# Performance work log

Hardware: AMD Instinct MI355X
Metric: run time of the kernel (lower is better)

Reference implementation:

```python
import jax, jax.numpy as jnp
import numpy as np

N = 4096       # nodes
NFEAT = 256    # feature dim
NCLASS = 16
E = 65536      # edges = N * avg_degree(16)
NLAYER = 4
ALPHA = 0.5    # blancealpha (non-trainable)
LAMBDA_1 = 1.0
LAMBDA_2 = 1.0
EPS = 1e-12    # F.normalize eps


def setup_inputs() -> dict:
    key = jax.random.key(0)
    ks = jax.random.split(key, 9)
    feat = jax.random.normal(ks[0], (N, NFEAT), dtype=jnp.float32)
    z0 = jax.random.uniform(ks[1], (N, NFEAT), dtype=jnp.float32)       # torch.rand init of z
    w1 = jax.random.uniform(ks[2], (N, N), dtype=jnp.float32)           # uniform_(0,1)
    EA = jax.random.uniform(ks[3], (N, N), dtype=jnp.float32)           # uniform_(0,1)
    w2_w = jax.random.normal(ks[4], (2 * NFEAT, NCLASS), dtype=jnp.float32) * 0.05
    w2_b = jnp.zeros((NCLASS,), dtype=jnp.float32)
    edge_i = jax.random.randint(ks[5], (E,), 0, N, dtype=jnp.int32)
    edge_j = jax.random.randint(ks[6], (E,), 0, N, dtype=jnp.int32)
    edge_val = jax.random.uniform(ks[7], (E,), dtype=jnp.float32)
    # dense adjacency from the sparse edge list (coalesce -> duplicate indices sum)
    adj = jnp.zeros((N, N), dtype=jnp.float32).at[edge_i, edge_j].add(edge_val)
    # w22 = ones with zeros at edge positions (as in __init__)
    w22 = jnp.ones((N, N), dtype=jnp.float32).at[edge_i, edge_j].set(0.0)
    return dict(feat=feat, z0=z0, w1=w1, EA=EA, w2_w=w2_w, w2_b=w2_b,
                adj=adj, w22=w22, edge_val=edge_val, edge_i=edge_i, edge_j=edge_j)


def reference(feat, z0, w1, EA, w2_w, w2_b, adj, w22, edge_val, edge_i, edge_j):
    n = feat.shape[0]
    y = feat                      # y starts as feat
    z = z0                        # torch.rand init, passed in for determinism
    EP = jnp.ones((n, n), dtype=feat.dtype)
    masked_EA = ALPHA * EA * w22  # constant across layers
    for _ in range(NLAYER):
        # dropout is identity in eval mode (training=False)
        A = adj * EP + masked_EA            # [n, n]
        yyT = y @ y.T                       # [n, n] (reused; same values as the two torch.mm calls)
        temp = EP.T @ y + A @ y - yyT @ y   # [n, nfeat]
        temp = jax.nn.sigmoid(w1 @ temp)
        y_n = (LAMBDA_2 / 2) * temp + feat
        z_n = z - A @ z                     # (I - A) @ z
        # ans(z, adj): edgewise ||z_i - z_j|| * adj_val scattered to dense
        P = jnp.linalg.norm(z[edge_i] - z[edge_j], axis=1) * edge_val   # [E]
        M = jnp.zeros((n, n), dtype=z.dtype).at[edge_i, edge_j].add(P)
        EP = (LAMBDA_2 * (yyT - masked_EA) - LAMBDA_1 * 0.5 * M) / LAMBDA_2
        y, z = y_n, z_n
    # F.normalize(p=2, dim=1)
    y = y / jnp.maximum(jnp.linalg.norm(y, axis=1, keepdims=True), EPS)
    z = z / jnp.maximum(jnp.linalg.norm(z, axis=1, keepdims=True), EPS)
    p = jnp.concatenate([z, y], axis=1)     # [n, 2*nfeat]
    logits = p @ w2_w + w2_b
    return jax.nn.log_softmax(logits, axis=1)
```

## Files before the change

### kernel.cpp

```cpp
#include <hip/hip_runtime.h>

#define Nn 4096
#define Ff 256
#define NCLS 16
#define Ne 65536
#define TSZ 262144
#define NF (Nn*Ff)
#define NNx (Nn*Nn)
#define KS 4

typedef unsigned short u16;
typedef unsigned int u32;
typedef __attribute__((ext_vector_type(8))) short short8;
typedef __attribute__((ext_vector_type(4))) float float4v;

__device__ __forceinline__ float bfh(u16 u){ return __uint_as_float(((u32)u)<<16); }
__device__ __forceinline__ u16 f2bf(float f){
    u32 u = __float_as_uint(f);
    return (u16)((u + 0x7FFFu + ((u>>16)&1u)) >> 16);
}
__device__ __forceinline__ void gload16(const u16* g, u16* l){
    __builtin_amdgcn_global_load_lds(
        (const __attribute__((address_space(1))) u32*)(const void*)g,
        (__attribute__((address_space(3))) u32*)(void*)l, 16, 0, 0);
}

__device__ float g_yA[NF], g_yB[NF], g_zA[NF], g_zB[NF], g_t1[NF], g_T1[NF];
__device__ float g_Gp[16*Ff*Ff], g_col[Ff], g_P[Ne], g_cc[Ne], g_hV[TSZ];
__device__ float g_pb[(size_t)KS*NF];
__device__ u32 g_hK[TSZ], g_slot[Ne];
__device__ int g_cntI[Nn], g_cntJ[Nn], g_rpI[Nn+1], g_rpJ[Nn+1], g_fI[Nn], g_fJ[Nn];
__device__ int g_lI[Ne], g_lJ[Ne];
__device__ __align__(16) u16 g_w1h[NNx], g_w1l[NNx];
__device__ __align__(16) u16 g_meh[NNx], g_mel[NNx];
__device__ __align__(16) u16 g_mth[NNx], g_mtl[NNx];
__device__ __align__(16) u16 g_x0h[NF], g_x0l[NF], g_x1h[NF], g_x1l[NF];
__device__ __align__(16) u16 g_zt0h[NF], g_zt0l[NF], g_zt1h[NF], g_zt1l[NF];
__device__ __align__(16) u16 g_yr0h[NF], g_yr0l[NF], g_yr1h[NF], g_yr1l[NF];
__device__ __align__(16) u16 g_tth[NF], g_ttl[NF];
__device__ __align__(16) u16 g_gth[Ff*Ff], g_gtl[Ff*Ff];

__global__ __launch_bounds__(256) void k_zero(float* p, int n){
    int i = blockIdx.x*256 + threadIdx.x;
    if (i < n) p[i] = 0.f;
}
__global__ __launch_bounds__(256) void k_zeroi(int* p, int n){
    int i = blockIdx.x*256 + threadIdx.x;
    if (i < n) p[i] = 0;
}
__global__ __launch_bounds__(256) void k_fillc(float* p, float v, int n){
    int i = blockIdx.x*256 + threadIdx.x;
    if (i < n) p[i] = v;
}
__global__ __launch_bounds__(256) void k_hkeys_clear(u32* K){
    int i = blockIdx.x*256 + threadIdx.x;
    if (i < TSZ) K[i] = 0xFFFFFFFFu;
}
__global__ __launch_bounds__(256) void k_hsetup(u32* K, u32* slot, const int* ei, const int* ej){
    int e = blockIdx.x*256 + threadIdx.x;
    if (e >= Ne) return;
    u32 key = ((u32)ei[e] << 12) | (u32)ej[e];
    u32 h = (key * 2654435761u) & (TSZ-1);
    for (;;){
        u32 old = atomicCAS(&K[h], 0xFFFFFFFFu, key);
        if (old == 0xFFFFFFFFu || old == key){ slot[e] = h; break; }
        h = (h+1) & (TSZ-1);
    }
}

__global__ __launch_bounds__(256) void k_count(int* cntI, int* cntJ, const int* ei, const int* ej){
    int e = blockIdx.x*256 + threadIdx.x;
    if (e < Ne){ atomicAdd(&cntI[ei[e]], 1); atomicAdd(&cntJ[ej[e]], 1); }
}
__global__ __launch_bounds__(1024) void k_scan(const int* cnt, int* rp){
    __shared__ int s[1024];
    int t = threadIdx.x, b = t*4;
    int a0 = cnt[b], a1 = cnt[b+1], a2 = cnt[b+2], a3 = cnt[b+3];
    int sum = a0+a1+a2+a3;
    s[t] = sum; __syncthreads();
    for (int o = 1; o < 1024; o <<= 1){
        int v = (t >= o) ? s[t-o] : 0;
        __syncthreads();
        s[t] += v;
        __syncthreads();
    }
    int excl = s[t] - sum;
    rp[b] = excl; rp[b+1] = excl+a0; rp[b+2] = excl+a0+a1; rp[b+3] = excl+a0+a1+a2;
    if (t == 1023) rp[4096] = s[1023];
}
__global__ __launch_bounds__(256) void k_fillcsr(const int* rpI, const int* rpJ, int* fI, int* fJ,
                                                 int* lI, int* lJ, const int* ei, const int* ej){
    int e = blockIdx.x*256 + threadIdx.x;
    if (e >= Ne) return;
    int i = ei[e], j = ej[e];
    lI[rpI[i] + atomicAdd(&fI[i], 1)] = e;
    lJ[rpJ[j] + atomicAdd(&fJ[j], 1)] = e;
}

__global__ __launch_bounds__(256) void k_split4(ushort4* hi, ushort4* lo, const float4* w, int n4){
    int i = blockIdx.x*256 + threadIdx.x;
    if (i >= n4) return;
    float4 v = w[i];
    ushort4 h, l;
    h.x = f2bf(v.x); l.x = f2bf(v.x - bfh(h.x));
    h.y = f2bf(v.y); l.y = f2bf(v.y - bfh(h.y));
    h.z = f2bf(v.z); l.z = f2bf(v.z - bfh(h.z));
    h.w = f2bf(v.w); l.w = f2bf(v.w - bfh(h.w));
    hi[i] = h; lo[i] = l;
}
__global__ __launch_bounds__(256) void k_splitME2(u16* meh, u16* mel, u16* mth, u16* mtl,
                                                  const float* ea, const float* w22){
    __shared__ float T[64][65];
    int r0 = blockIdx.y*64, c0 = blockIdx.x*64;
    int c4 = threadIdx.x & 15, rr = threadIdx.x >> 4;
    for (int q = 0; q < 4; ++q){
        int r = q*16 + rr;
        size_t idx = (size_t)(r0+r)*Nn + c0 + c4*4;
        float4 e4 = *(const float4*)(ea + idx);
        float4 w4 = *(const float4*)(w22 + idx);
        float v0 = 0.5f*e4.x*w4.x, v1 = 0.5f*e4.y*w4.y, v2 = 0.5f*e4.z*w4.z, v3 = 0.5f*e4.w*w4.w;
        ushort4 h, l;
        h.x = f2bf(v0); l.x = f2bf(v0 - bfh(h.x));
        h.y = f2bf(v1); l.y = f2bf(v1 - bfh(h.y));
        h.z = f2bf(v2); l.z = f2bf(v2 - bfh(h.z));
        h.w = f2bf(v3); l.w = f2bf(v3 - bfh(h.w));
        *(ushort4*)(meh + idx) = h; *(ushort4*)(mel + idx) = l;
        T[r][c4*4+0] = v0; T[r][c4*4+1] = v1; T[r][c4*4+2] = v2; T[r][c4*4+3] = v3;
    }
    __syncthreads();
    for (int q = 0; q < 4; ++q){
        int oc = q*16 + rr;
        float v0 = T[c4*4+0][oc], v1 = T[c4*4+1][oc], v2 = T[c4*4+2][oc], v3 = T[c4*4+3][oc];
        ushort4 h, l;
        h.x = f2bf(v0); l.x = f2bf(v0 - bfh(h.x));
        h.y = f2bf(v1); l.y = f2bf(v1 - bfh(h.y));
        h.z = f2bf(v2); l.z = f2bf(v2 - bfh(h.z));
        h.w = f2bf(v3); l.w = f2bf(v3 - bfh(h.w));
        size_t o = (size_t)(c0+oc)*Nn + r0 + c4*4;
        *(ushort4*)(mth + o) = h; *(ushort4*)(mtl + o) = l;
    }
}
__global__ __launch_bounds__(256) void k_splitXT(u16* hi, u16* lo, const float* X){
    __shared__ float T[64][65];
    int r0 = blockIdx.y*64, c0 = blockIdx.x*64;
    int c = threadIdx.x & 63, rr = threadIdx.x >> 6;
    for (int q = 0; q < 16; ++q){
        int r = q*4 + rr;
        T[r][c] = X[(size_t)(r0+r)*Ff + c0 + c];
    }
    __syncthreads();
    for (int q = 0; q < 16; ++q){
        int r = q*4 + rr;
        float v = T[c][r];
        size_t o = (size_t)(c0+r)*Nn + r0 + c;
        u16 h = f2bf(v); hi[o] = h; lo[o] = f2bf(v - bfh(h));
    }
}
__global__ __launch_bounds__(256) void k_splitGT(u16* hi, u16* lo, const float* Gp){
    __shared__ float T[64][65];
    int r0 = blockIdx.y*64, c0 = blockIdx.x*64;
    int c = threadIdx.x & 63, rr = threadIdx.x >> 6;
    for (int q = 0; q < 16; ++q){
        int r = q*4 + rr;
        float v = 0.f;
        #pragma unroll
        for (int z = 0; z < 16; ++z) v += Gp[z*(Ff*Ff) + (r0+r)*Ff + c0 + c];
        T[r][c] = v;
    }
    __syncthreads();
    for (int q = 0; q < 16; ++q){
        int r = q*4 + rr;
        float v = T[c][r];
        int o = (c0+r)*Ff + r0 + c;
        u16 h = f2bf(v); hi[o] = h; lo[o] = f2bf(v - bfh(h));
    }
}

__device__ __forceinline__ void mm_tile(
    const u16* __restrict__ Ahp, const u16* __restrict__ Alp,
    const u16* __restrict__ Bhp, const u16* __restrict__ Blp,
    size_t sA, size_t sB, int i0, int j0, int k0,
    u16* LAh, u16* LAl, u16* LBh, u16* LBl,
    float4v* acc, int lane, int w)
{
    const int g1 = w*64 + lane;
    const int g2 = g1 + 256;
    const int r1 = g1>>3, p1 = g1&7, r2 = g2>>3, p2 = g2&7;
    const size_t a1 = (size_t)(i0+r1)*sA + (size_t)(k0 + ((p1 ^ (r1&7))<<3));
    const size_t a2 = (size_t)(i0+r2)*sA + (size_t)(k0 + ((p2 ^ (r2&7))<<3));
    const size_t b1 = (size_t)(j0+r1)*sB + (size_t)(k0 + ((p1 ^ (r1&7))<<3));
    const size_t b2 = (size_t)(j0+r2)*sB + (size_t)(k0 + ((p2 ^ (r2&7))<<3));
    __syncthreads();
    gload16(Ahp + a1, LAh + g1*8);
    gload16(Ahp + a2, LAh + g2*8);
    gload16(Alp + a1, LAl + g1*8);
    gload16(Alp + a2, LAl + g2*8);
    gload16(Bhp + b1, LBh + g1*8);
    gload16(Bhp + b2, LBh + g2*8);
    gload16(Blp + b1, LBl + g1*8);
    gload16(Blp + b2, LBl + g2*8);
    __syncthreads();
    const int arow = w*16 + (lane&15);
    const int aswz = arow & 7;
    #pragma unroll
    for (int kk = 0; kk < 2; ++kk){
        const int ch = kk*4 + (lane>>4);
        short8 ah = *(const short8*)(LAh + arow*64 + ((ch ^ aswz)<<3));
        short8 al = *(const short8*)(LAl + arow*64 + ((ch ^ aswz)<<3));
        #pragma unroll
        for (int c = 0; c < 4; ++c){
            const int brow = c*16 + (lane&15);
            const int bo = brow*64 + ((ch ^ (brow&7))<<3);
            short8 bh = *(const short8*)(LBh + bo);
            short8 bl = *(const short8*)(LBl + bo);
            acc[c] = __builtin_amdgcn_mfma_f32_16x16x32_bf16(ah, bh, acc[c], 0,0,0);
            acc[c] = __builtin_amdgcn_mfma_f32_16x16x32_bf16(ah, bl, acc[c], 0,0,0);
            acc[c] = __builtin_amdgcn_mfma_f32_16x16x32_bf16(al, bh, acc[c], 0,0,0);
        }
    }
}

template<int V>
__global__ __launch_bounds__(256) void k_mm(float* __restrict__ out,
        const u16* __restrict__ Ahp, const u16* __restrict__ Alp,
        const u16* __restrict__ Bhp, const u16* __restrict__ Blp,
        const float* __restrict__ aux1){
    __shared__ u16 LAh[4096], LAl[4096], LBh[4096], LBl[4096];
    const int tid = threadIdx.x, lane = tid & 63, w = tid >> 6;
    const int j0 = blockIdx.x*64, i0 = blockIdx.y*64;
    float4v acc[4];
    #pragma unroll
    for (int c = 0; c < 4; ++c) acc[c] = (float4v){0.f,0.f,0.f,0.f};
    for (int kt = 0; kt < 4; ++kt)
        mm_tile(Ahp, Alp, Bhp, Blp, (size_t)Ff, (size_t)Ff, i0, j0, kt*64, LAh, LAl, LBh, LBl, acc, lane, w);
    #pragma unroll
    for (int c = 0; c < 4; ++c)
        #pragma unroll
        for (int r = 0; r < 4; ++r){
            int grow = i0 + w*16 + (lane>>4)*4 + r;
            int gcol = j0 + c*16 + (lane&15);
            size_t idx = (size_t)grow*Ff + gcol;
            float v = acc[c][r];
            if constexpr (V == 3) out[idx] = aux1[idx] - v;
            if constexpr (V == 4) out[idx] = aux1[gcol] - v;
            if constexpr (V == 5) out[idx] = v;
        }
}

__global__ __launch_bounds__(256) void k_gram_mm(float* __restrict__ Gp,
        const u16* __restrict__ Ahp, const u16* __restrict__ Alp,
        const u16* __restrict__ Bhp, const u16* __restrict__ Blp){
    __shared__ u16 LAh[4096], LAl[4096], LBh[4096], LBl[4096];
    const int tid = threadIdx.x, lane = tid & 63, w = tid >> 6;
    const int j0 = blockIdx.x*64, i0 = blockIdx.y*64, kb = blockIdx.z*256;
    float4v acc[4];
    #pragma unroll
    for (int c = 0; c < 4; ++c) acc[c] = (float4v){0.f,0.f,0.f,0.f};
    for (int kt = 0; kt < 4; ++kt)
        mm_tile(Ahp, Alp, Bhp, Blp, (size_t)Nn, (size_t)Nn, i0, j0, kb + kt*64, LAh, LAl, LBh, LBl, acc, lane, w);
    float* op = Gp + (size_t)blockIdx.z*(Ff*Ff);
    #pragma unroll
    for (int c = 0; c < 4; ++c)
        #pragma unroll
        for (int r = 0; r < 4; ++r){
            int grow = i0 + w*16 + (lane>>4)*4 + r;
            int gcol = j0 + c*16 + (lane&15);
            op[grow*Ff + gcol] = acc[c][r];
        }
}

__global__ __launch_bounds__(512) void k_mmB(float* __restrict__ pb,
        const u16* __restrict__ Ah, const u16* __restrict__ Al,
        const u16* __restrict__ Bh, const u16* __restrict__ Bl){
    __shared__ u16 LA[2][2][8192];
    __shared__ u16 LB[2][2][8192];
    const int tid = threadIdx.x, lane = tid & 63, w = tid >> 6;
    const int j0 = blockIdx.x*128, i0 = blockIdx.y*128;
    const int kbase = blockIdx.z*1024;
    const int wr = w >> 1, wc = w & 1;
    float4v acc[2][4];
    #pragma unroll
    for (int m = 0; m < 2; ++m)
        #pragma unroll
        for (int n = 0; n < 4; ++n) acc[m][n] = (float4v){0.f,0.f,0.f,0.f};

    const int srow = tid >> 3, sp = tid & 7;
    const size_t aoff0 = (size_t)(i0 + srow)*Nn + (size_t)((sp ^ (srow&7))<<3);
    const size_t aoff1 = aoff0 + (size_t)64*Nn;
    const size_t boff0 = (size_t)(j0 + srow)*Nn + (size_t)((sp ^ (srow&7))<<3);
    const size_t boff1 = boff0 + (size_t)64*Nn;
    const int d0 = tid*8, d1 = tid*8 + 4096;

#define STAGE(B, K0) { \
    gload16(Ah + aoff0 + (K0), &LA[B][0][d0]); \
    gload16(Ah + aoff1 + (K0), &LA[B][0][d1]); \
    gload16(Al + aoff0 + (K0), &LA[B][1][d0]); \
    gload16(Al + aoff1 + (K0), &LA[B][1][d1]); \
    gload16(Bh + boff0 + (K0), &LB[B][0][d0]); \
    gload16(Bh + boff1 + (K0), &LB[B][0][d1]); \
    gload16(Bl + boff0 + (K0), &LB[B][1][d0]); \
    gload16(Bl + boff1 + (K0), &LB[B][1][d1]); }

#define COMPUTE(B) { \
    _Pragma("unroll") \
    for (int kk = 0; kk < 2; ++kk){ \
        const int ch = kk*4 + (lane>>4); \
        short8 ah0, al0, ah1, al1; \
        { int ar = wr*32 + (lane&15); int ao = ar*64 + ((ch ^ (ar&7))<<3); \
          ah0 = *(const short8*)&LA[B][0][ao]; al0 = *(const short8*)&LA[B][1][ao]; } \
        { int ar = wr*32 + 16 + (lane&15); int ao = ar*64 + ((ch ^ (ar&7))<<3); \
          ah1 = *(const short8*)&LA[B][0][ao]; al1 = *(const short8*)&LA[B][1][ao]; } \
        _Pragma("unroll") \
        for (int n = 0; n < 4; ++n){ \
            int bc = wc*64 + n*16 + (lane&15); int bo = bc*64 + ((ch ^ (bc&7))<<3); \
            short8 bh = *(const short8*)&LB[B][0][bo]; \
            short8 bl = *(const short8*)&LB[B][1][bo]; \
            acc[0][n] = __builtin_amdgcn_mfma_f32_16x16x32_bf16(ah0, bh, acc[0][n], 0,0,0); \
            acc[0][n] = __builtin_amdgcn_mfma_f32_16x16x32_bf16(ah0, bl, acc[0][n], 0,0,0); \
            acc[0][n] = __builtin_amdgcn_mfma_f32_16x16x32_bf16(al0, bh, acc[0][n], 0,0,0); \
            acc[1][n] = __builtin_amdgcn_mfma_f32_16x16x32_bf16(ah1, bh, acc[1][n], 0,0,0); \
            acc[1][n] = __builtin_amdgcn_mfma_f32_16x16x32_bf16(ah1, bl, acc[1][n], 0,0,0); \
            acc[1][n] = __builtin_amdgcn_mfma_f32_16x16x32_bf16(al1, bh, acc[1][n], 0,0,0); \
        } \
    } }

    STAGE(0, kbase)
    __syncthreads();
    for (int kt = 0; kt < 16; ++kt){
        if (kt < 15) STAGE((kt+1)&1, kbase + (kt+1)*64)
        COMPUTE(kt&1)
        __syncthreads();
    }
#undef STAGE
#undef COMPUTE

    float* op = pb + (size_t)blockIdx.z*NF;
    #pragma unroll
    for (int m = 0; m < 2; ++m)
        #pragma unroll
        for (int n = 0; n < 4; ++n)
            #pragma unroll
            for (int r = 0; r < 4; ++r){
                int row = i0 + wr*32 + m*16 + (lane>>4)*4 + r;
                int col = j0 + wc*64 + n*16 + (lane&15);
                op[(size_t)row*Ff + col] = acc[m][n][r];
            }
}

template<int V, int DOSPLIT>
__global__ __launch_bounds__(256) void k_redT(float* __restrict__ out, const float* __restrict__ pb,
        const float* __restrict__ aux, u16* __restrict__ rh, u16* __restrict__ rl,
        u16* __restrict__ th, u16* __restrict__ tl){
    __shared__ float T[64][65];
    const int c0 = blockIdx.x*64, r0 = blockIdx.y*64;
    const int c = threadIdx.x & 63, rr = threadIdx.x >> 6;
    for (int q = 0; q < 16; ++q){
        int row = q*4 + rr;
        size_t idx = (size_t)(r0+row)*Ff + c0 + c;
        float s = pb[idx] + pb[NF+idx] + pb[2*(size_t)NF+idx] + pb[3*(size_t)NF+idx];
        float val;
        if constexpr (V == 0) val = out[idx] + s;
        if constexpr (V == 1) val = out[idx] - s;
        if constexpr (V == 2) val = aux[idx] + 0.5f*(1.f/(1.f+expf(-s)));
        if constexpr (V == 3) val = aux[idx] - s;
        out[idx] = val;
        if constexpr (V == 2){
            u16 h = f2bf(val); rh[idx] = h; rl[idx] = f2bf(val - bfh(h));
        }
        if constexpr (DOSPLIT) T[row][c] = val;
    }
    if constexpr (DOSPLIT){
        __syncthreads();
        for (int q = 0; q < 16; ++q){
            int r = q*4 + rr;
            float v = T[c][r];
            size_t o = (size_t)(c0+r)*Nn + r0 + c;
            u16 h = f2bf(v); th[o] = h; tl[o] = f2bf(v - bfh(h));
        }
    }
}

__global__ __launch_bounds__(256) void k_csrTZ(float* __restrict__ t1, float* __restrict__ zn,
        const float* __restrict__ y, const float* __restrict__ z,
        const float* __restrict__ cc, const float* __restrict__ P,
        const int* __restrict__ rpI, const int* __restrict__ lI, const int* __restrict__ ej,
        const int* __restrict__ rpJ, const int* __restrict__ lJ, const int* __restrict__ ei,
        int useM){
    const int r = blockIdx.x, f = threadIdx.x;
    float at = 0.f, az = 0.f;
    const int b0 = rpI[r], b1 = rpI[r+1];
    for (int p = b0; p < b1; ++p){
        int e = lI[p];
        float ce = cc[e];
        int j = ej[e];
        at += ce * y[(size_t)j*Ff + f];
        az += ce * z[(size_t)j*Ff + f];
    }
    if (useM){
        const int c0 = rpJ[r], c1 = rpJ[r+1];
        for (int p = c0; p < c1; ++p){
            int e = lJ[p];
            at -= 0.5f * P[e] * y[(size_t)ei[e]*Ff + f];
        }
    }
    t1[(size_t)r*Ff + f] += at;
    zn[(size_t)r*Ff + f] -= az;
}

__global__ __launch_bounds__(256) void k_colsum(float* col, const float* __restrict__ y){
    int j = threadIdx.x;
    int r0 = blockIdx.x*64;
    float s = 0.f;
    for (int i = 0; i < 64; ++i) s += y[(size_t)(r0+i)*Ff + j];
    atomicAdd(&col[j], s);
}

__global__ __launch_bounds__(256) void k_pacc(float* __restrict__ P, float* __restrict__ hV,
        const float* __restrict__ z, const int* __restrict__ ei, const int* __restrict__ ej,
        const float* __restrict__ ev, const u32* __restrict__ slot){
    int e = blockIdx.x*4 + (threadIdx.x >> 6);
    int lane = threadIdx.x & 63;
    int i = ei[e], j = ej[e];
    float s = 0.f;
    #pragma unroll
    for (int q = 0; q < 4; ++q){
        int f = lane + q*64;
        float d = z[(size_t)i*Ff + f] - z[(size_t)j*Ff + f];
        s += d*d;
    }
    #pragma unroll
    for (int o = 32; o; o >>= 1) s += __shfl_xor(s, o);
    if (lane == 0){
        float v = sqrtf(s) * ev[e];
        P[e] = v;
        atomicAdd(&hV[slot[e]], v);
    }
}
__global__ __launch_bounds__(256) void k_ep(float* __restrict__ c, const float* __restrict__ y,
        const int* __restrict__ ei, const int* __restrict__ ej, const float* __restrict__ ev,
        const float* __restrict__ V, const u32* __restrict__ slot){
    int e = blockIdx.x*4 + (threadIdx.x >> 6);
    int lane = threadIdx.x & 63;
    int i = ei[e], j = ej[e];
    float s = 0.f;
    #pragma unroll
    for (int q = 0; q < 4; ++q){
        int f = lane + q*64;
        s += y[(size_t)i*Ff + f] * y[(size_t)j*Ff + f];
    }
    #pragma unroll
    for (int o = 32; o; o >>= 1) s += __shfl_xor(s, o);
    if (lane == 0) c[e] = ev[e] * (s - 0.5f * V[slot[e]]);
}

__global__ __launch_bounds__(256) void k_head(float* __restrict__ out, const float* __restrict__ y,
                                              const float* __restrict__ z, const float* __restrict__ w2w,
                                              const float* __restrict__ w2b){
    const int node = blockIdx.x, t = threadIdx.x;
    float yv = y[(size_t)node*Ff + t], zv = z[(size_t)node*Ff + t];
    float yc = fminf(fmaxf(yv, -1e37f), 1e37f);
    float zc = fminf(fmaxf(zv, -1e37f), 1e37f);
    __shared__ float sy[256], sz[256];
    sy[t] = fabsf(yc); sz[t] = fabsf(zc);
    __syncthreads();
    for (int s = 128; s; s >>= 1){ if (t < s){ sy[t]=fmaxf(sy[t],sy[t+s]); sz[t]=fmaxf(sz[t],sz[t+s]); } __syncthreads(); }
    float my_ = fmaxf(sy[0], 1e-30f), mz_ = fmaxf(sz[0], 1e-30f);
    __syncthreads();
    float ysc = yc/my_, zsc = zc/mz_;
    sy[t] = ysc*ysc; sz[t] = zsc*zsc;
    __syncthreads();
    for (int s = 128; s; s >>= 1){ if (t < s){ sy[t]+=sy[t+s]; sz[t]+=sz[t+s]; } __syncthreads(); }
    float ny = fmaxf(my_*sqrtf(sy[0]), 1e-12f);
    float nz = fmaxf(mz_*sqrtf(sz[0]), 1e-12f);
    float ynv = yc/ny, znv = zc/nz;
    float acc[NCLS];
    #pragma unroll
    for (int cc = 0; cc < NCLS; ++cc)
        acc[cc] = znv*w2w[t*NCLS+cc] + ynv*w2w[(Ff+t)*NCLS+cc];
    __shared__ float red[NCLS][257];
    #pragma unroll
    for (int cc = 0; cc < NCLS; ++cc) red[cc][t] = acc[cc];
    __syncthreads();
    for (int s = 128; s; s >>= 1){
        if (t < s){
            #pragma unroll
            for (int cc = 0; cc < NCLS; ++cc) red[cc][t] += red[cc][t+s];
        }
        __syncthreads();
    }
    __shared__ float lg[NCLS];
    __shared__ float ml[2];
    if (t < NCLS) lg[t] = red[t][0] + w2b[t];
    __syncthreads();
    if (t == 0){
        float m = -1e30f;
        for (int cc = 0; cc < NCLS; ++cc) m = fmaxf(m, lg[cc]);
        float se = 0.f;
        for (int cc = 0; cc < NCLS; ++cc) se += expf(lg[cc]-m);
        ml[0] = m; ml[1] = logf(se);
    }
    __syncthreads();
    if (t < NCLS) out[(size_t)node*NCLS + t] = lg[t] - ml[0] - ml[1];
}

extern "C" void kernel_launch(void* const* d_in, const int* in_sizes, int n_in,
                              void* d_out, int out_size, void* d_ws, size_t ws_size,
                              hipStream_t stream){
    const float* feat = (const float*)d_in[0];
    const float* z0i  = (const float*)d_in[1];
    const float* w1p  = (const float*)d_in[2];
    const float* EAp  = (const float*)d_in[3];
    const float* w2w  = (const float*)d_in[4];
    const float* w2b  = (const float*)d_in[5];
    const float* w22p = (const float*)d_in[7];
    const float* evp  = (const float*)d_in[8];
    const int* ei   = (const int*)d_in[9];
    const int* ej   = (const int*)d_in[10];
    float* out = (float*)d_out;

    int ok = (n_in == 11) && (out_size == Nn*NCLS)
           && in_sizes[0]==NF && in_sizes[1]==NF && in_sizes[2]==NNx && in_sizes[3]==NNx
           && in_sizes[4]==2*Ff*NCLS && in_sizes[5]==NCLS && in_sizes[6]==NNx && in_sizes[7]==NNx
           && in_sizes[8]==Ne && in_sizes[9]==Ne && in_sizes[10]==Ne;
    if (!ok){
        k_fillc<<<(out_size+255)/256, 256, 0, stream>>>(out, -100.0f, out_size);
        return;
    }

    float *yA,*yB,*zA,*zB,*t1,*T1,*Gp,*col,*P,*cc,*hV,*pb; u32 *hK,*slot;
    int *cntI,*cntJ,*rpI,*rpJ,*fI,*fJ,*lI,*lJ;
    u16 *w1h,*w1l,*meh,*mel,*mth,*mtl,*gth,*gtl,*tth,*ttl;
    u16 *xh[2],*xl[2],*zth[2],*ztl[2],*yrh[2],*yrl[2];
    hipGetSymbolAddress((void**)&yA,  HIP_SYMBOL(g_yA));
    hipGetSymbolAddress((void**)&yB,  HIP_SYMBOL(g_yB));
    hipGetSymbolAddress((void**)&zA,  HIP_SYMBOL(g_zA));
    hipGetSymbolAddress((void**)&zB,  HIP_SYMBOL(g_zB));
    hipGetSymbolAddress((void**)&t1,  HIP_SYMBOL(g_t1));
    hipGetSymbolAddress((void**)&T1,  HIP_SYMBOL(g_T1));
    hipGetSymbolAddress((void**)&Gp,  HIP_SYMBOL(g_Gp));
    hipGetSymbolAddress((void**)&col, HIP_SYMBOL(g_col));
    hipGetSymbolAddress((void**)&P,   HIP_SYMBOL(g_P));
    hipGetSymbolAddress((void**)&cc,  HIP_SYMBOL(g_cc));
    hipGetSymbolAddress((void**)&hV,  HIP_SYMBOL(g_hV));
    hipGetSymbolAddress((void**)&pb,  HIP_SYMBOL(g_pb));
    hipGetSymbolAddress((void**)&hK,  HIP_SYMBOL(g_hK));
    hipGetSymbolAddress((void**)&slot,HIP_SYMBOL(g_slot));
    hipGetSymbolAddress((void**)&cntI,HIP_SYMBOL(g_cntI));
    hipGetSymbolAddress((void**)&cntJ,HIP_SYMBOL(g_cntJ));
    hipGetSymbolAddress((void**)&rpI, HIP_SYMBOL(g_rpI));
    hipGetSymbolAddress((void**)&rpJ, HIP_SYMBOL(g_rpJ));
    hipGetSymbolAddress((void**)&fI,  HIP_SYMBOL(g_fI));
    hipGetSymbolAddress((void**)&fJ,  HIP_SYMBOL(g_fJ));
    hipGetSymbolAddress((void**)&lI,  HIP_SYMBOL(g_lI));
    hipGetSymbolAddress((void**)&lJ,  HIP_SYMBOL(g_lJ));
    hipGetSymbolAddress((void**)&w1h, HIP_SYMBOL(g_w1h));
    hipGetSymbolAddress((void**)&w1l, HIP_SYMBOL(g_w1l));
    hipGetSymbolAddress((void**)&meh, HIP_SYMBOL(g_meh));
    hipGetSymbolAddress((void**)&mel, HIP_SYMBOL(g_mel));
    hipGetSymbolAddress((void**)&mth, HIP_SYMBOL(g_mth));
    hipGetSymbolAddress((void**)&mtl, HIP_SYMBOL(g_mtl));
    hipGetSymbolAddress((void**)&gth, HIP_SYMBOL(g_gth));
    hipGetSymbolAddress((void**)&gtl, HIP_SYMBOL(g_gtl));
    hipGetSymbolAddress((void**)&tth, HIP_SYMBOL(g_tth));
    hipGetSymbolAddress((void**)&ttl, HIP_SYMBOL(g_ttl));
    hipGetSymbolAddress((void**)&xh[0], HIP_SYMBOL(g_x0h));
    hipGetSymbolAddress((void**)&xl[0], HIP_SYMBOL(g_x0l));
    hipGetSymbolAddress((void**)&xh[1], HIP_SYMBOL(g_x1h));
    hipGetSymbolAddress((void**)&xl[1], HIP_SYMBOL(g_x1l));
    hipGetSymbolAddress((void**)&zth[0], HIP_SYMBOL(g_zt0h));
    hipGetSymbolAddress((void**)&ztl[0], HIP_SYMBOL(g_zt0l));
    hipGetSymbolAddress((void**)&zth[1], HIP_SYMBOL(g_zt1h));
    hipGetSymbolAddress((void**)&ztl[1], HIP_SYMBOL(g_zt1l));
    hipGetSymbolAddress((void**)&yrh[0], HIP_SYMBOL(g_yr0h));
    hipGetSymbolAddress((void**)&yrl[0], HIP_SYMBOL(g_yr0l));
    hipGetSymbolAddress((void**)&yrh[1], HIP_SYMBOL(g_yr1h));
    hipGetSymbolAddress((void**)&yrl[1], HIP_SYMBOL(g_yr1l));

    const dim3 gSmall(Ff/64, Nn/64);
    const dim3 gXT(Ff/64, Nn/64);
    const dim3 gME(Nn/64, Nn/64);
    const dim3 gGT(Ff/64, Ff/64);
    const dim3 gGram(4, 4, 16);
    const dim3 gB(2, Nn/128, KS);
    const dim3 gRed(Ff/64, Nn/64);

    k_split4<<<NNx/4/256, 256, 0, stream>>>((ushort4*)w1h, (ushort4*)w1l, (const float4*)w1p, NNx/4);
    k_splitME2<<<gME, 256, 0, stream>>>(meh, mel, mth, mtl, EAp, w22p);
    k_split4<<<NF/4/256, 256, 0, stream>>>((ushort4*)yrh[0], (ushort4*)yrl[0], (const float4*)feat, NF/4);
    k_splitXT<<<gXT, 256, 0, stream>>>(xh[0], xl[0], feat);
    k_splitXT<<<gXT, 256, 0, stream>>>(zth[0], ztl[0], z0i);
    k_hkeys_clear<<<TSZ/256, 256, 0, stream>>>(hK);
    k_hsetup<<<Ne/256, 256, 0, stream>>>(hK, slot, ei, ej);
    k_zeroi<<<Nn/256, 256, 0, stream>>>(cntI, Nn);
    k_zeroi<<<Nn/256, 256, 0, stream>>>(cntJ, Nn);
    k_count<<<Ne/256, 256, 0, stream>>>(cntI, cntJ, ei, ej);
    k_scan<<<1, 1024, 0, stream>>>(cntI, rpI);
    k_scan<<<1, 1024, 0, stream>>>(cntJ, rpJ);
    k_zeroi<<<Nn/256, 256, 0, stream>>>(fI, Nn);
    k_zeroi<<<Nn/256, 256, 0, stream>>>(fJ, Nn);
    k_fillcsr<<<Ne/256, 256, 0, stream>>>(rpI, rpJ, fI, fJ, lI, lJ, ei, ej);

    const float* yv = feat;  const float* zv = z0i;
    for (int t = 1; t <= 4; ++t){
        int ri = (t-1) & 1, wi = t & 1;
        u16 *xhc = xh[ri], *xlc = xl[ri], *xhn = xh[wi], *xln = xl[wi];
        u16 *zthc = zth[ri], *ztlc = ztl[ri], *zthn = zth[wi], *ztln = ztl[wi];
        u16 *yrhc = yrh[ri], *yrlc = yrl[ri], *yrhn = yrh[wi], *yrln = yrl[wi];
        float* yn = (t & 1) ? yA : yB;
        float* zn = (t & 1) ? zA : zB;
        const float* ccv = (t == 1) ? evp : cc;

        k_gram_mm<<<gGram, 256, 0, stream>>>(Gp, xhc, xlc, xhc, xlc);
        k_splitGT<<<gGT, 256, 0, stream>>>(gth, gtl, Gp);
        if (t == 1){
            k_zero<<<1, 256, 0, stream>>>(col, Ff);
            k_colsum<<<64, 256, 0, stream>>>(col, yv);
            k_mm<4><<<gSmall, 256, 0, stream>>>(t1, yrhc, yrlc, gth, gtl, col);
        } else {
            k_mm<3><<<gSmall, 256, 0, stream>>>(t1, yrhc, yrlc, gth, gtl, T1);
        }
        k_mmB<<<gB, 512, 0, stream>>>(pb, meh, mel, zthc, ztlc);
        k_redT<3,0><<<gRed, 256, 0, stream>>>(zn, pb, zv, nullptr, nullptr, nullptr, nullptr);
        k_csrTZ<<<Nn, 256, 0, stream>>>(t1, zn, yv, zv, ccv, P, rpI, lI, ej, rpJ, lJ, ei, (t >= 2) ? 1 : 0);
        if (t < 4)
            k_splitXT<<<gXT, 256, 0, stream>>>(zthn, ztln, zn);
        k_mmB<<<gB, 512, 0, stream>>>(pb, meh, mel, xhc, xlc);
        if (t == 1){
            k_redT<0,1><<<gRed, 256, 0, stream>>>(t1, pb, nullptr, nullptr, nullptr, tth, ttl);
        } else {
            k_redT<0,0><<<gRed, 256, 0, stream>>>(t1, pb, nullptr, nullptr, nullptr, nullptr, nullptr);
            k_mmB<<<gB, 512, 0, stream>>>(pb, mth, mtl, xhc, xlc);
            k_redT<1,1><<<gRed, 256, 0, stream>>>(t1, pb, nullptr, nullptr, nullptr, tth, ttl);
        }
        k_mmB<<<gB, 512, 0, stream>>>(pb, w1h, w1l, tth, ttl);
        k_redT<2,1><<<gRed, 256, 0, stream>>>(yn, pb, feat, yrhn, yrln, xhn, xln);
        if (t < 4){
            k_zero<<<TSZ/256, 256, 0, stream>>>(hV, TSZ);
            k_pacc<<<Ne/4, 256, 0, stream>>>(P, hV, zv, ei, ej, evp, slot);
            k_ep<<<Ne/4, 256, 0, stream>>>(cc, yv, ei, ej, evp, hV, slot);
            k_gram_mm<<<gGram, 256, 0, stream>>>(Gp, xhc, xlc, xhn, xln);
            k_splitGT<<<gGT, 256, 0, stream>>>(gth, gtl, Gp);
            k_mm<5><<<gSmall, 256, 0, stream>>>(T1, yrhc, yrlc, gth, gtl, nullptr);
        }
        yv = yn; zv = zn;
    }
    k_head<<<Nn, 256, 0, stream>>>(out, yv, zv, w2w, w2b);
}
```

Measured before the change: 1.568 ms.

## Batch the three big N×N×F GEMMs into one launch with full-width tiles

Restructures k_mmB so each block computes a 64x256 output tile (all feature columns) with split-K of 8. A z-dimension selects among up to three independent GEMMs (ME·x, ME·z, MEᵀ·x), so they run in one launch instead of sequentially. The z-update reduction is folded into k_csrTZ and the per-product reductions into new k_redT1/k_redY kernels, which removes several launches and partial-buffer passes. The cost is a single-buffered LDS pipeline with no prefetch, a 3x larger partial-sum buffer, more partial reads per reduction, and a scalarised k_splitME2 setup kernel.

```diff
diff --git a/kernel.cpp b/kernel.cpp
--- a/kernel.cpp
+++ b/kernel.cpp
@@ -7,7 +7,7 @@
 #define TSZ 262144
 #define NF (Nn*Ff)
 #define NNx (Nn*Nn)
-#define KS 4
+#define KS 8
 
 typedef unsigned short u16;
 typedef unsigned int u32;
@@ -27,7 +27,7 @@
 
 __device__ float g_yA[NF], g_yB[NF], g_zA[NF], g_zB[NF], g_t1[NF], g_T1[NF];
 __device__ float g_Gp[16*Ff*Ff], g_col[Ff], g_P[Ne], g_cc[Ne], g_hV[TSZ];
-__device__ float g_pb[(size_t)KS*NF];
+__device__ float g_pb[(size_t)3*KS*NF];
 __device__ u32 g_hK[TSZ], g_slot[Ne];
 __device__ int g_cntI[Nn], g_cntJ[Nn], g_rpI[Nn+1], g_rpJ[Nn+1], g_fI[Nn], g_fJ[Nn];
 __device__ int g_lI[Ne], g_lJ[Ne];
@@ -112,32 +112,20 @@
                                                   const float* ea, const float* w22){
     __shared__ float T[64][65];
     int r0 = blockIdx.y*64, c0 = blockIdx.x*64;
-    int c4 = threadIdx.x & 15, rr = threadIdx.x >> 4;
-    for (int q = 0; q < 4; ++q){
-        int r = q*16 + rr;
-        size_t idx = (size_t)(r0+r)*Nn + c0 + c4*4;
-        float4 e4 = *(const float4*)(ea + idx);
-        float4 w4 = *(const float4*)(w22 + idx);
-        float v0 = 0.5f*e4.x*w4.x, v1 = 0.5f*e4.y*w4.y, v2 = 0.5f*e4.z*w4.z, v3 = 0.5f*e4.w*w4.w;
-        ushort4 h, l;
-        h.x = f2bf(v0); l.x = f2bf(v0 - bfh(h.x));
-        h.y = f2bf(v1); l.y = f2bf(v1 - bfh(h.y));
-        h.z = f2bf(v2); l.z = f2bf(v2 - bfh(h.z));
-        h.w = f2bf(v3); l.w = f2bf(v3 - bfh(h.w));
-        *(ushort4*)(meh + idx) = h; *(ushort4*)(mel + idx) = l;
-        T[r][c4*4+0] = v0; T[r][c4*4+1] = v1; T[r][c4*4+2] = v2; T[r][c4*4+3] = v3;
-    }
-    __syncthreads();
-    for (int q = 0; q < 4; ++q){
-        int oc = q*16 + rr;
-        float v0 = T[c4*4+0][oc], v1 = T[c4*4+1][oc], v2 = T[c4*4+2][oc], v3 = T[c4*4+3][oc];
-        ushort4 h, l;
-        h.x = f2bf(v0); l.x = f2bf(v0 - bfh(h.x));
-        h.y = f2bf(v1); l.y = f2bf(v1 - bfh(h.y));
-        h.z = f2bf(v2); l.z = f2bf(v2 - bfh(h.z));
-        h.w = f2bf(v3); l.w = f2bf(v3 - bfh(h.w));
-        size_t o = (size_t)(c0+oc)*Nn + r0 + c4*4;
-        *(ushort4*)(mth + o) = h; *(ushort4*)(mtl + o) = l;
+    int c = threadIdx.x & 63, rr = threadIdx.x >> 6;
+    for (int q = 0; q < 16; ++q){
+        int r = q*4 + rr;
+        size_t idx = (size_t)(r0+r)*Nn + c0 + c;
+        float v = 0.5f*ea[idx]*w22[idx];
+        T[r][c] = v;
+        u16 h = f2bf(v); meh[idx] = h; mel[idx] = f2bf(v - bfh(h));
+    }
+    __syncthreads();
+    for (int q = 0; q < 16; ++q){
+        int r = q*4 + rr;
+        float v = T[c][r];
+        size_t o = (size_t)(c0+r)*Nn + r0 + c;
+        u16 h = f2bf(v); mth[o] = h; mtl[o] = f2bf(v - bfh(h));
     }
 }
 __global__ __launch_bounds__(256) void k_splitXT(u16* hi, u16* lo, const float* X){
@@ -270,71 +258,75 @@
 }
 
 __global__ __launch_bounds__(512) void k_mmB(float* __restrict__ pb,
-        const u16* __restrict__ Ah, const u16* __restrict__ Al,
-        const u16* __restrict__ Bh, const u16* __restrict__ Bl){
-    __shared__ u16 LA[2][2][8192];
-    __shared__ u16 LB[2][2][8192];
+        const u16* __restrict__ A0h, const u16* __restrict__ A0l,
+        const u16* __restrict__ B0h, const u16* __restrict__ B0l,
+        const u16* __restrict__ A1h, const u16* __restrict__ A1l,
+        const u16* __restrict__ B1h, const u16* __restrict__ B1l,
+        const u16* __restrict__ A2h, const u16* __restrict__ A2l,
+        const u16* __restrict__ B2h, const u16* __restrict__ B2l){
+    __shared__ u16 LAh[4096], LAl[4096], LBh[16384], LBl[16384];
     const int tid = threadIdx.x, lane = tid & 63, w = tid >> 6;
-    const int j0 = blockIdx.x*128, i0 = blockIdx.y*128;
-    const int kbase = blockIdx.z*1024;
-    const int wr = w >> 1, wc = w & 1;
+    const int z = blockIdx.x, i0 = blockIdx.y*64, bat = blockIdx.z;
+    const u16 *Ah, *Al, *Bh, *Bl;
+    if (bat == 0){ Ah = A0h; Al = A0l; Bh = B0h; Bl = B0l; }
+    else if (bat == 1){ Ah = A1h; Al = A1l; Bh = B1h; Bl = B1l; }
+    else { Ah = A2h; Al = A2l; Bh = B2h; Bl = B2l; }
+    const int wr = w >> 2, wc = w & 3;
     float4v acc[2][4];
     #pragma unroll
     for (int m = 0; m < 2; ++m)
         #pragma unroll
         for (int n = 0; n < 4; ++n) acc[m][n] = (float4v){0.f,0.f,0.f,0.f};
 
-    const int srow = tid >> 3, sp = tid & 7;
-    const size_t aoff0 = (size_t)(i0 + srow)*Nn + (size_t)((sp ^ (srow&7))<<3);
-    const size_t aoff1 = aoff0 + (size_t)64*Nn;
-    const size_t boff0 = (size_t)(j0 + srow)*Nn + (size_t)((sp ^ (srow&7))<<3);
-    const size_t boff1 = boff0 + (size_t)64*Nn;
-    const int d0 = tid*8, d1 = tid*8 + 4096;
-
-#define STAGE(B, K0) { \
-    gload16(Ah + aoff0 + (K0), &LA[B][0][d0]); \
-    gload16(Ah + aoff1 + (K0), &LA[B][0][d1]); \
-    gload16(Al + aoff0 + (K0), &LA[B][1][d0]); \
-    gload16(Al + aoff1 + (K0), &LA[B][1][d1]); \
-    gload16(Bh + boff0 + (K0), &LB[B][0][d0]); \
-    gload16(Bh + boff1 + (K0), &LB[B][0][d1]); \
-    gload16(Bl + boff0 + (K0), &LB[B][1][d0]); \
-    gload16(Bl + boff1 + (K0), &LB[B][1][d1]); }
-
-#define COMPUTE(B) { \
-    _Pragma("unroll") \
-    for (int kk = 0; kk < 2; ++kk){ \
-        const int ch = kk*4 + (lane>>4); \
-        short8 ah0, al0, ah1, al1; \
-        { int ar = wr*32 + (lane&15); int ao = ar*64 + ((ch ^ (ar&7))<<3); \
-          ah0 = *(const short8*)&LA[B][0][ao]; al0 = *(const short8*)&LA[B][1][ao]; } \
-        { int ar = wr*32 + 16 + (lane&15); int ao = ar*64 + ((ch ^ (ar&7))<<3); \
-          ah1 = *(const short8*)&LA[B][0][ao]; al1 = *(const short8*)&LA[B][1][ao]; } \
-        _Pragma("unroll") \
-        for (int n = 0; n < 4; ++n){ \
-            int bc = wc*64 + n*16 + (lane&15); int bo = bc*64 + ((ch ^ (bc&7))<<3); \
-            short8 bh = *(const short8*)&LB[B][0][bo]; \
-            short8 bl = *(const short8*)&LB[B][1][bo]; \
-            acc[0][n] = __builtin_amdgcn_mfma_f32_16x16x32_bf16(ah0, bh, acc[0][n], 0,0,0); \
-            acc[0][n] = __builtin_amdgcn_mfma_f32_16x16x32_bf16(ah0, bl, acc[0][n], 0,0,0); \
-            acc[0][n] = __builtin_amdgcn_mfma_f32_16x16x32_bf16(al0, bh, acc[0][n], 0,0,0); \
-            acc[1][n] = __builtin_amdgcn_mfma_f32_16x16x32_bf16(ah1, bh, acc[1][n], 0,0,0); \
-            acc[1][n] = __builtin_amdgcn_mfma_f32_16x16x32_bf16(ah1, bl, acc[1][n], 0,0,0); \
-            acc[1][n] = __builtin_amdgcn_mfma_f32_16x16x32_bf16(al1, bh, acc[1][n], 0,0,0); \
-        } \
-    } }
-
-    STAGE(0, kbase)
-    __syncthreads();
-    for (int kt = 0; kt < 16; ++kt){
-        if (kt < 15) STAGE((kt+1)&1, kbase + (kt+1)*64)
-        COMPUTE(kt&1)
+    const int ra = tid >> 3, pa = tid & 7;
+    const size_t aoff = (size_t)(i0+ra)*Nn + (size_t)((pa ^ (ra&7))<<3);
+
+    for (int kt = 0; kt < 8; ++kt){
+        const int k0 = z*512 + kt*64;
         __syncthreads();
-    }
-#undef STAGE
-#undef COMPUTE
-
-    float* op = pb + (size_t)blockIdx.z*NF;
+        gload16(Ah + aoff + k0, LAh + tid*8);
+        gload16(Al + aoff + k0, LAl + tid*8);
+        #pragma unroll
+        for (int it = 0; it < 4; ++it){
+            int g = it*512 + tid;
+            int r = g >> 3, p = g & 7;
+            size_t b = (size_t)r*Nn + (size_t)(k0 + ((p ^ (r&7))<<3));
+            gload16(Bh + b, LBh + g*8);
+            gload16(Bl + b, LBl + g*8);
+        }
+        __syncthreads();
+        #pragma unroll
+        for (int kk = 0; kk < 2; ++kk){
+            const int ch = kk*4 + (lane>>4);
+            short8 ah0, ah1, al0, al1;
+            {
+                const int arow = wr*32 + (lane&15);
+                const int ao = arow*64 + ((ch ^ (arow&7))<<3);
+                ah0 = *(const short8*)(LAh + ao);
+                al0 = *(const short8*)(LAl + ao);
+            }
+            {
+                const int arow = wr*32 + 16 + (lane&15);
+                const int ao = arow*64 + ((ch ^ (arow&7))<<3);
+                ah1 = *(const short8*)(LAh + ao);
+                al1 = *(const short8*)(LAl + ao);
+            }
+            #pragma unroll
+            for (int n = 0; n < 4; ++n){
+                const int bcol = wc*64 + n*16 + (lane&15);
+                const int bo = bcol*64 + ((ch ^ (bcol&7))<<3);
+                short8 bh = *(const short8*)(LBh + bo);
+                short8 bl = *(const short8*)(LBl + bo);
+                acc[0][n] = __builtin_amdgcn_mfma_f32_16x16x32_bf16(ah0, bh, acc[0][n], 0,0,0);
+                acc[0][n] = __builtin_amdgcn_mfma_f32_16x16x32_bf16(ah0, bl, acc[0][n], 0,0,0);
+                acc[0][n] = __builtin_amdgcn_mfma_f32_16x16x32_bf16(al0, bh, acc[0][n], 0,0,0);
+                acc[1][n] = __builtin_amdgcn_mfma_f32_16x16x32_bf16(ah1, bh, acc[1][n], 0,0,0);
+                acc[1][n] = __builtin_amdgcn_mfma_f32_16x16x32_bf16(ah1, bl, acc[1][n], 0,0,0);
+                acc[1][n] = __builtin_amdgcn_mfma_f32_16x16x32_bf16(al1, bh, acc[1][n], 0,0,0);
+            }
+        }
+    }
+    float* op = pb + ((size_t)bat*KS + z)*NF;
     #pragma unroll
     for (int m = 0; m < 2; ++m)
         #pragma unroll
@@ -342,14 +334,13 @@
             #pragma unroll
             for (int r = 0; r < 4; ++r){
                 int row = i0 + wr*32 + m*16 + (lane>>4)*4 + r;
-                int col = j0 + wc*64 + n*16 + (lane&15);
+                int col = wc*64 + n*16 + (lane&15);
                 op[(size_t)row*Ff + col] = acc[m][n][r];
             }
 }
 
-template<int V, int DOSPLIT>
-__global__ __launch_bounds__(256) void k_redT(float* __restrict__ out, const float* __restrict__ pb,
-        const float* __restrict__ aux, u16* __restrict__ rh, u16* __restrict__ rl,
+template<int HASM, int DOSPLIT>
+__global__ __launch_bounds__(256) void k_redT1(float* __restrict__ t1, const float* __restrict__ pb,
         u16* __restrict__ th, u16* __restrict__ tl){
     __shared__ float T[64][65];
     const int c0 = blockIdx.x*64, r0 = blockIdx.y*64;
@@ -357,16 +348,15 @@
     for (int q = 0; q < 16; ++q){
         int row = q*4 + rr;
         size_t idx = (size_t)(r0+row)*Ff + c0 + c;
-        float s = pb[idx] + pb[NF+idx] + pb[2*(size_t)NF+idx] + pb[3*(size_t)NF+idx];
-        float val;
-        if constexpr (V == 0) val = out[idx] + s;
-        if constexpr (V == 1) val = out[idx] - s;
-        if constexpr (V == 2) val = aux[idx] + 0.5f*(1.f/(1.f+expf(-s)));
-        if constexpr (V == 3) val = aux[idx] - s;
-        out[idx] = val;
-        if constexpr (V == 2){
-            u16 h = f2bf(val); rh[idx] = h; rl[idx] = f2bf(val - bfh(h));
-        }
+        float s = 0.f;
+        #pragma unroll
+        for (int p = 0; p < KS; ++p) s += pb[(size_t)p*NF + idx];
+        if constexpr (HASM){
+            #pragma unroll
+            for (int p = 0; p < KS; ++p) s -= pb[((size_t)2*KS + p)*NF + idx];
+        }
+        float val = t1[idx] + s;
+        t1[idx] = val;
         if constexpr (DOSPLIT) T[row][c] = val;
     }
     if constexpr (DOSPLIT){
@@ -380,8 +370,34 @@
     }
 }
 
+__global__ __launch_bounds__(256) void k_redY(float* __restrict__ yn, const float* __restrict__ pb,
+        const float* __restrict__ feat, u16* __restrict__ rh, u16* __restrict__ rl,
+        u16* __restrict__ th, u16* __restrict__ tl){
+    __shared__ float T[64][65];
+    const int c0 = blockIdx.x*64, r0 = blockIdx.y*64;
+    const int c = threadIdx.x & 63, rr = threadIdx.x >> 6;
+    for (int q = 0; q < 16; ++q){
+        int row = q*4 + rr;
+        size_t idx = (size_t)(r0+row)*Ff + c0 + c;
+        float s = 0.f;
+        #pragma unroll
+        for (int p = 0; p < KS; ++p) s += pb[(size_t)p*NF + idx];
+        float val = feat[idx] + 0.5f*(1.f/(1.f+expf(-s)));
+        yn[idx] = val;
+        u16 h = f2bf(val); rh[idx] = h; rl[idx] = f2bf(val - bfh(h));
+        T[row][c] = val;
+    }
+    __syncthreads();
+    for (int q = 0; q < 16; ++q){
+        int r = q*4 + rr;
+        float v = T[c][r];
+        size_t o = (size_t)(c0+r)*Nn + r0 + c;
+        u16 h = f2bf(v); th[o] = h; tl[o] = f2bf(v - bfh(h));
+    }
+}
+
 __global__ __launch_bounds__(256) void k_csrTZ(float* __restrict__ t1, float* __restrict__ zn,
-        const float* __restrict__ y, const float* __restrict__ z,
+        const float* __restrict__ y, const float* __restrict__ z, const float* __restrict__ pb1,
         const float* __restrict__ cc, const float* __restrict__ P,
         const int* __restrict__ rpI, const int* __restrict__ lI, const int* __restrict__ ej,
         const int* __restrict__ rpJ, const int* __restrict__ lJ, const int* __restrict__ ei,
@@ -403,8 +419,12 @@
             at -= 0.5f * P[e] * y[(size_t)ei[e]*Ff + f];
         }
     }
-    t1[(size_t)r*Ff + f] += at;
-    zn[(size_t)r*Ff + f] -= az;
+    size_t idx = (size_t)r*Ff + f;
+    float dz = 0.f;
+    #pragma unroll
+    for (int p = 0; p < KS; ++p) dz += pb1[(size_t)p*NF + idx];
+    t1[idx] += at;
+    zn[idx] = z[idx] - dz - az;
 }
 
 __global__ __launch_bounds__(256) void k_colsum(float* col, const float* __restrict__ y){
@@ -581,7 +601,6 @@
     const dim3 gME(Nn/64, Nn/64);
     const dim3 gGT(Ff/64, Ff/64);
     const dim3 gGram(4, 4, 16);
-    const dim3 gB(2, Nn/128, KS);
     const dim3 gRed(Ff/64, Nn/64);
 
     k_split4<<<NNx/4/256, 256, 0, stream>>>((ushort4*)w1h, (ushort4*)w1l, (const float4*)w1p, NNx/4);
@@ -619,21 +638,28 @@
         } else {
             k_mm<3><<<gSmall, 256, 0, stream>>>(t1, yrhc, yrlc, gth, gtl, T1);
         }
-        k_mmB<<<gB, 512, 0, stream>>>(pb, meh, mel, zthc, ztlc);
-        k_redT<3,0><<<gRed, 256, 0, stream>>>(zn, pb, zv, nullptr, nullptr, nullptr, nullptr);
-        k_csrTZ<<<Nn, 256, 0, stream>>>(t1, zn, yv, zv, ccv, P, rpI, lI, ej, rpJ, lJ, ei, (t >= 2) ? 1 : 0);
+        {
+            int nb = (t == 1) ? 2 : 3;
+            dim3 gB(KS, Nn/64, nb);
+            k_mmB<<<gB, 512, 0, stream>>>(pb,
+                meh, mel, xhc, xlc,
+                meh, mel, zthc, ztlc,
+                mth, mtl, xhc, xlc);
+        }
+        k_csrTZ<<<Nn, 256, 0, stream>>>(t1, zn, yv, zv, pb + (size_t)KS*NF, ccv, P,
+                                        rpI, lI, ej, rpJ, lJ, ei, (t >= 2) ? 1 : 0);
+        if (t == 1) k_redT1<0,1><<<gRed, 256, 0, stream>>>(t1, pb, tth, ttl);
+        else        k_redT1<1,1><<<gRed, 256, 0, stream>>>(t1, pb, tth, ttl);
         if (t < 4)
             k_splitXT<<<gXT, 256, 0, stream>>>(zthn, ztln, zn);
-        k_mmB<<<gB, 512, 0, stream>>>(pb, meh, mel, xhc, xlc);
-        if (t == 1){
-            k_redT<0,1><<<gRed, 256, 0, stream>>>(t1, pb, nullptr, nullptr, nullptr, tth, ttl);
-        } else {
-            k_redT<0,0><<<gRed, 256, 0, stream>>>(t1, pb, nullptr, nullptr, nullptr, nullptr, nullptr);
-            k_mmB<<<gB, 512, 0, stream>>>(pb, mth, mtl, xhc, xlc);
-            k_redT<1,1><<<gRed, 256, 0, stream>>>(t1, pb, nullptr, nullptr, nullptr, tth, ttl);
-        }
-        k_mmB<<<gB, 512, 0, stream>>>(pb, w1h, w1l, tth, ttl);
-        k_redT<2,1><<<gRed, 256, 0, stream>>>(yn, pb, feat, yrhn, yrln, xhn, xln);
+        {
+            dim3 gB(KS, Nn/64, 1);
+            k_mmB<<<gB, 512, 0, stream>>>(pb,
+                w1h, w1l, tth, ttl,
+                w1h, w1l, tth, ttl,
+                w1h, w1l, tth, ttl);
+        }
+        k_redY<<<gRed, 256, 0, stream>>>(yn, pb, feat, yrhn, yrln, xhn, xln);
         if (t < 4){
             k_zero<<<TSZ/256, 256, 0, stream>>>(hV, TSZ);
             k_pacc<<<Ne/4, 256, 0, stream>>>(P, hV, zv, ei, ej, evp, slot);
```

Result: faster. 1.479 ms (-5.7%).
